# Optimization experiments

Hardware: AMD Instinct MI355X
Metric: run time of the kernel (lower is better)

## Reference

```python
import jax, jax.numpy as jnp
import numpy as np

D, H, DFF, MD = 1024, 16, 4096, 128
B, TS, TT = 8, 512, 512
EPS = 1e-6


def _ln(x, s, b):
    m = jnp.mean(x, axis=-1, keepdims=True)
    v = jnp.mean((x - m) ** 2, axis=-1, keepdims=True)
    return (x - m) * jax.lax.rsqrt(v + EPS) * s + b


def _rel_bias(emb, qlen, klen):
    # T5-style bidirectional bucket: [H, qlen, klen]
    q = jnp.arange(qlen)[:, None]
    k = jnp.arange(klen)[None, :]
    rp = k - q
    bucket = jnp.where(rp < 0, jnp.minimum(-rp, MD - 1), jnp.minimum(rp, MD - 1) + MD)
    return emb[bucket].transpose(2, 0, 1)


def _mha(xq, xkv, w_in, b_in, w_out, b_out, bias):
    # nn.MultiheadAttention math: packed in_proj [3D,D], additive attn bias [H,Tq,Tk]
    Bq, Tq, _ = xq.shape
    Tk = xkv.shape[1]
    hd = D // H
    wq, wk, wv = jnp.split(w_in, 3, axis=0)
    bq, bk, bv = jnp.split(b_in, 3, axis=0)
    q = (xq @ wq.T + bq).reshape(Bq, Tq, H, hd).transpose(0, 2, 1, 3)
    k = (xkv @ wk.T + bk).reshape(Bq, Tk, H, hd).transpose(0, 2, 1, 3)
    v = (xkv @ wv.T + bv).reshape(Bq, Tk, H, hd).transpose(0, 2, 1, 3)
    scores = jnp.einsum('bhqd,bhkd->bhqk', q, k) / jnp.sqrt(jnp.asarray(hd, xq.dtype))
    scores = scores + bias[None]
    attn = jax.nn.softmax(scores, axis=-1)
    out = jnp.einsum('bhqk,bhkd->bhqd', attn, v)
    out = out.transpose(0, 2, 1, 3).reshape(Bq, Tq, D)
    return out @ w_out.T + b_out


def setup_inputs() -> dict:
    key = jax.random.key(0)
    ks = jax.random.split(key, 40)
    std = 0.02

    def n(i, shape):
        return jax.random.normal(ks[i], shape, dtype=jnp.float32) * std

    return {
        'src': jax.random.normal(ks[0], (B, TS, D), dtype=jnp.float32),
        'tgt': jax.random.normal(ks[1], (B, TT, D), dtype=jnp.float32),
        # encoder layer
        'enc_in_w': n(2, (3 * D, D)), 'enc_in_b': jnp.zeros((3 * D,)),
        'enc_out_w': n(3, (D, D)), 'enc_out_b': jnp.zeros((D,)),
        'enc_ff1_w': n(4, (DFF, D)), 'enc_ff1_b': jnp.zeros((DFF,)),
        'enc_ff2_w': n(5, (D, DFF)), 'enc_ff2_b': jnp.zeros((D,)),
        'enc_n1_s': jnp.ones((D,)), 'enc_n1_b': jnp.zeros((D,)),
        'enc_n2_s': jnp.ones((D,)), 'enc_n2_b': jnp.zeros((D,)),
        'enc_rel': n(6, (2 * MD, H)),
        # decoder layer
        'dec_sa_in_w': n(7, (3 * D, D)), 'dec_sa_in_b': jnp.zeros((3 * D,)),
        'dec_sa_out_w': n(8, (D, D)), 'dec_sa_out_b': jnp.zeros((D,)),
        'dec_ca_in_w': n(9, (3 * D, D)), 'dec_ca_in_b': jnp.zeros((3 * D,)),
        'dec_ca_out_w': n(10, (D, D)), 'dec_ca_out_b': jnp.zeros((D,)),
        'dec_ff1_w': n(11, (DFF, D)), 'dec_ff1_b': jnp.zeros((DFF,)),
        'dec_ff2_w': n(12, (D, DFF)), 'dec_ff2_b': jnp.zeros((D,)),
        'dec_n1_s': jnp.ones((D,)), 'dec_n1_b': jnp.zeros((D,)),
        'dec_n2_s': jnp.ones((D,)), 'dec_n2_b': jnp.zeros((D,)),
        'dec_n3_s': jnp.ones((D,)), 'dec_n3_b': jnp.zeros((D,)),
        'dec_rel_self': n(13, (2 * MD, H)),
        'dec_rel_cross': n(14, (2 * MD, H)),
    }


def reference(src, tgt,
              enc_in_w, enc_in_b, enc_out_w, enc_out_b,
              enc_ff1_w, enc_ff1_b, enc_ff2_w, enc_ff2_b,
              enc_n1_s, enc_n1_b, enc_n2_s, enc_n2_b, enc_rel,
              dec_sa_in_w, dec_sa_in_b, dec_sa_out_w, dec_sa_out_b,
              dec_ca_in_w, dec_ca_in_b, dec_ca_out_w, dec_ca_out_b,
              dec_ff1_w, dec_ff1_b, dec_ff2_w, dec_ff2_b,
              dec_n1_s, dec_n1_b, dec_n2_s, dec_n2_b, dec_n3_s, dec_n3_b,
              dec_rel_self, dec_rel_cross):
    Ts, Tt = src.shape[1], tgt.shape[1]

    # ---- encoder layer (pre-LN) ----
    eb = _rel_bias(enc_rel, Ts, Ts)  # [H,Ts,Ts]
    x = src
    x = x + _mha(_ln(x, enc_n1_s, enc_n1_b), _ln(x, enc_n1_s, enc_n1_b),
                 enc_in_w, enc_in_b, enc_out_w, enc_out_b, eb)
    h = _ln(x, enc_n2_s, enc_n2_b)
    x = x + (jax.nn.relu(h @ enc_ff1_w.T + enc_ff1_b) @ enc_ff2_w.T + enc_ff2_b)
    memory = x

    # ---- decoder layer (pre-LN) ----
    causal = jnp.where(jnp.arange(Tt)[None, :] > jnp.arange(Tt)[:, None], -jnp.inf, 0.0)
    sb = _rel_bias(dec_rel_self, Tt, Tt) + causal[None]  # [H,Tt,Tt]
    cb = _rel_bias(dec_rel_cross, Tt, Ts)                # [H,Tt,Ts]
    y = tgt
    yn = _ln(y, dec_n1_s, dec_n1_b)
    y = y + _mha(yn, yn, dec_sa_in_w, dec_sa_in_b, dec_sa_out_w, dec_sa_out_b, sb)
    y = y + _mha(_ln(y, dec_n2_s, dec_n2_b), memory,
                 dec_ca_in_w, dec_ca_in_b, dec_ca_out_w, dec_ca_out_b, cb)
    h = _ln(y, dec_n3_s, dec_n3_b)
    y = y + (jax.nn.relu(h @ dec_ff1_w.T + dec_ff1_b) @ dec_ff2_w.T + dec_ff2_b)
    return y
```

## Files before the change

### kernel.cpp

```cpp
#include <hip/hip_runtime.h>

using u16 = unsigned short;

typedef float f32x4 __attribute__((ext_vector_type(4)));
typedef __bf16 bf16x8v __attribute__((ext_vector_type(8)));
typedef bf16x8v bf16x8 __attribute__((may_alias));
typedef u16 u16x8v __attribute__((ext_vector_type(8)));
typedef u16x8v u16x8 __attribute__((may_alias));
typedef u16 u16x4v __attribute__((ext_vector_type(4)));
typedef u16x4v u16x4 __attribute__((may_alias));
typedef float f32x4v __attribute__((ext_vector_type(4)));
typedef f32x4v float4a __attribute__((may_alias));

#define GPTR(p) ((__attribute__((address_space(1))) void*)(p))
#define LPTR(p) ((__attribute__((address_space(3))) void*)(p))

__device__ __forceinline__ u16 f2bf(float f) {
  unsigned u = __builtin_bit_cast(unsigned, f);
  u += 0x7FFFu + ((u >> 16) & 1u);
  return (u16)(u >> 16);
}

__device__ __forceinline__ f32x4 mfma16(bf16x8 a, bf16x8 b, f32x4 c) {
  return __builtin_amdgcn_mfma_f32_16x16x32_bf16(a, b, c, 0, 0, 0);
}

struct Srcs { const float* s[10]; };

__global__ __launch_bounds__(256) void cvt_all(Srcs srcs, u16* __restrict__ dst) {
  constexpr int off[11] = {0, 786432, 1048576, 2097152, 3145728,
                           3932160, 4194304, 4980736, 5242880, 6291456, 7340032};
  const int i = blockIdx.x * 256 + threadIdx.x;
  int r = 0;
#pragma unroll
  for (int j = 1; j < 10; j++) r += (i >= off[j]);
  float4a v = ((const float4a*)srcs.s[r])[i - off[r]];
  u16x4 o;
  o[0] = f2bf(v[0]); o[1] = f2bf(v[1]); o[2] = f2bf(v[2]); o[3] = f2bf(v[3]);
  ((u16x4*)dst)[i] = o;
}

__global__ __launch_bounds__(256) void add_cvt(const float* __restrict__ a,
                                               const float* __restrict__ b,
                                               u16* __restrict__ o) {
  const int i = blockIdx.x * 256 + threadIdx.x;
  float4a va = ((const float4a*)a)[i];
  float4a vb = ((const float4a*)b)[i];
  u16x4 ov;
#pragma unroll
  for (int j = 0; j < 4; j++) ov[j] = f2bf(va[j] + vb[j]);
  ((u16x4*)o)[i] = ov;
}

__global__ __launch_bounds__(256) void add_f32(float* __restrict__ o,
                                               const float* __restrict__ b) {
  const int i = blockIdx.x * 256 + threadIdx.x;
  float4a vo = ((float4a*)o)[i];
  float4a vb = ((const float4a*)b)[i];
#pragma unroll
  for (int j = 0; j < 4; j++) vo[j] += vb[j];
  ((float4a*)o)[i] = vo;
}

__global__ __launch_bounds__(256) void ln_k(const float* __restrict__ x,
                                            const float* __restrict__ sc,
                                            const float* __restrict__ bi,
                                            u16* __restrict__ out) {
  const int row = blockIdx.x, tid = threadIdx.x;
  float4a v = ((const float4a*)(x + (size_t)row * 1024))[tid];
  float s1 = v[0] + v[1] + v[2] + v[3];
  float s2 = v[0]*v[0] + v[1]*v[1] + v[2]*v[2] + v[3]*v[3];
#pragma unroll
  for (int off = 32; off; off >>= 1) { s1 += __shfl_xor(s1, off); s2 += __shfl_xor(s2, off); }
  __shared__ float red[8];
  if ((tid & 63) == 0) { red[tid >> 6] = s1; red[4 + (tid >> 6)] = s2; }
  __syncthreads();
  s1 = red[0] + red[1] + red[2] + red[3];
  s2 = red[4] + red[5] + red[6] + red[7];
  const float mean = s1 * (1.f / 1024.f);
  const float rstd = rsqrtf(s2 * (1.f / 1024.f) - mean * mean + 1e-6f);
  float4a s4 = ((const float4a*)sc)[tid];
  float4a b4 = ((const float4a*)bi)[tid];
  u16x4 o;
#pragma unroll
  for (int j = 0; j < 4; j++) o[j] = f2bf((v[j] - mean) * rstd * s4[j] + b4[j]);
  ((u16x4*)(out + (size_t)row * 1024))[tid] = o;
}

template <int BN_T, int MW, int EPI, int PF>
__global__ __launch_bounds__(256) void gemm_bt(
    const u16* __restrict__ A, int lda,
    const u16* __restrict__ W, int ldw,
    const float* __restrict__ bias,
    const float* __restrict__ C0, int ldc0,
    void* __restrict__ outv, int ldo, int K,
    float* __restrict__ part) {
  constexpr int BM = 128, BK = 64;
  constexpr int NW = 4 / MW;
  constexpr int FM = BM / MW / 16;
  constexpr int FN = BN_T / NW / 16;
  constexpr int RA = (BM * BK * 2) / 4096;
  constexpr int RB = (BN_T * BK * 2) / 4096;
  constexpr int NB = PF ? 2 : 1;
  __shared__ alignas(16) u16 As[NB][BM * BK];
  __shared__ alignas(16) u16 Bs[NB][BN_T * BK];
  const int tid = threadIdx.x, lane = tid & 63, wv = tid >> 6;
  const int kb = (EPI == 3) ? blockIdx.z * K : 0;

  const int gx = gridDim.x;
  const int nwg = gx * gridDim.y;
  const int orig = blockIdx.y * gx + blockIdx.x;
  const int qq = nwg >> 3, rr = nwg & 7;
  const int xcd = orig & 7, idx = orig >> 3;
  const int wg = (xcd < rr ? xcd * (qq + 1) : rr * (qq + 1) + (xcd - rr) * qq) + idx;
  const int bm = (wg / gx) * BM, bn = (wg % gx) * BN_T;

  const int wr = (wv / NW) * (BM / MW);
  const int wc = (wv % NW) * (BN_T / NW);
  const int la = lane & 15, lg = lane >> 4;
  const int r7 = la & 7;
  const int srow = wv * 8 + (lane >> 3);
  const int scol = ((lane & 7) ^ (lane >> 3)) << 3;
  const u16* gA = A + (size_t)(bm + srow) * lda + scol;
  const u16* gB = W + (size_t)(bn + srow) * ldw + scol;

  f32x4 acc[FM][FN] = {};

  auto stage = [&](int buf, int k0) {
#pragma unroll
    for (int r = 0; r < RA; r++)
      __builtin_amdgcn_global_load_lds(GPTR(gA + (size_t)r * 32 * lda + k0),
                                       LPTR(&As[buf][(wv * 8 + r * 32) * BK]), 16, 0, 0);
#pragma unroll
    for (int r = 0; r < RB; r++)
      __builtin_amdgcn_global_load_lds(GPTR(gB + (size_t)r * 32 * ldw + k0),
                                       LPTR(&Bs[buf][(wv * 8 + r * 32) * BK]), 16, 0, 0);
  };

  auto compute = [&](int buf) {
#pragma unroll
    for (int kk = 0; kk < BK; kk += 32) {
      const int off = ((((kk >> 3) + lg) ^ r7) << 3);
      bf16x8 af[FM], bfr[FN];
#pragma unroll
      for (int m = 0; m < FM; m++)
        af[m] = *(const bf16x8*)&As[buf][(wr + m * 16 + la) * BK + off];
#pragma unroll
      for (int n = 0; n < FN; n++)
        bfr[n] = *(const bf16x8*)&Bs[buf][(wc + n * 16 + la) * BK + off];
#pragma unroll
      for (int m = 0; m < FM; m++)
#pragma unroll
        for (int n = 0; n < FN; n++)
          acc[m][n] = mfma16(af[m], bfr[n], acc[m][n]);
    }
  };

  if constexpr (PF) {
    stage(0, kb);
    int buf = 0;
    const int NT = K / BK;
    for (int t = 0; t < NT; ++t) {
      if (t + 1 < NT) {
        stage(buf ^ 1, kb + (t + 1) * BK);
        if constexpr (RA + RB == 8)
          asm volatile("s_waitcnt vmcnt(8)" ::: "memory");
        else
          asm volatile("s_waitcnt vmcnt(6)" ::: "memory");
      } else {
        asm volatile("s_waitcnt vmcnt(0)" ::: "memory");
      }
      __builtin_amdgcn_s_barrier();
      __builtin_amdgcn_sched_barrier(0);
      compute(buf);
      __builtin_amdgcn_s_barrier();
      buf ^= 1;
    }
  } else {
    for (int k0 = 0; k0 < K; k0 += BK) {
      __syncthreads();
      stage(0, kb + k0);
      __syncthreads();
      compute(0);
    }
  }

  const bool addb = (EPI != 3) || (blockIdx.z == 0);
  float bv[FN];
#pragma unroll
  for (int n = 0; n < FN; n++) bv[n] = addb ? bias[bn + wc + n * 16 + la] : 0.f;
#pragma unroll
  for (int m = 0; m < FM; m++) {
#pragma unroll
    for (int j = 0; j < 4; j++) {
      const int row = bm + wr + m * 16 + (lane >> 4) * 4 + j;
#pragma unroll
      for (int n = 0; n < FN; n++) {
        const int col = bn + wc + n * 16 + la;
        float v = acc[m][n][j] + bv[n];
        if constexpr (EPI == 1) v = fmaxf(v, 0.f);
        if constexpr (EPI == 2) {
          ((float*)outv)[(size_t)row * ldo + col] = v + C0[(size_t)row * ldc0 + col];
        } else if constexpr (EPI == 3) {
          if (blockIdx.z == 0)
            ((float*)outv)[(size_t)row * ldo + col] = v + C0[(size_t)row * ldc0 + col];
          else
            part[(size_t)row * ldo + col] = v;
        } else {
          ((u16*)outv)[(size_t)row * ldo + col] = f2bf(v);
        }
      }
    }
  }
}

template <bool CAUSAL>
__global__ __launch_bounds__(256) void attn_k(
    const u16* __restrict__ Qb, int ldq,
    const u16* __restrict__ Kb, int ldk,
    const u16* __restrict__ Vb, int ldv,
    const float* __restrict__ rel,
    u16* __restrict__ Ob, int ldo,
    int Tq, int Tk) {
  __shared__ alignas(16) u16 Ks[128 * 64];
  __shared__ alignas(16) u16 Vt[64 * 136];
  __shared__ alignas(16) u16 Ps[4][16 * 40];
  __shared__ float biasl[256];
  const int tid = threadIdx.x, lane = tid & 63, w = tid >> 6;
  const int b = blockIdx.y >> 4, h = blockIdx.y & 15;
  const int q0 = blockIdx.x * 64;
  const int la = lane & 15, lg = lane >> 4, r7 = la & 7;

  biasl[tid] = rel[tid * 16 + h];

  const int qr0 = q0 + w * 16;
  const u16* qp = Qb + (size_t)(b * Tq + qr0 + la) * ldq + h * 64 + lg * 8;
  const bf16x8 qf0 = *(const bf16x8*)qp;
  const bf16x8 qf1 = *(const bf16x8*)(qp + 32);

  float sm[4] = {0.f, 0.f, 0.f, 0.f};
  f32x4 acc[4] = {};

  const int kv_end = CAUSAL ? (q0 + 64) : Tk;
  const int scolK = ((lane & 7) ^ (lane >> 3)) << 3;
  const u16* gK = Kb + (size_t)(b * Tk + w * 8 + (lane >> 3)) * ldk + h * 64 + scolK;
  const int vrow = tid >> 3;
  const int vcol = (tid & 7) * 8;
  const int vsw = (tid & 3) * 8;
  const u16* gV = Vb + (size_t)(b * Tk + vrow) * ldv + h * 64 + vcol;
  u16* Pw = Ps[w];

  for (int kv0 = 0; kv0 < kv_end; kv0 += 128) {
    __syncthreads();
#pragma unroll
    for (int r = 0; r < 4; r++)
      __builtin_amdgcn_global_load_lds(GPTR(gK + (size_t)(kv0 + r * 32) * ldk),
                                       LPTR(&Ks[(w * 8 + r * 32) * 64]), 16, 0, 0);
    u16x8 vreg[4];
#pragma unroll
    for (int r = 0; r < 4; r++)
      vreg[r] = *(const u16x8*)(gV + (size_t)(kv0 + r * 32) * ldv);
    asm volatile("s_waitcnt vmcnt(0)" ::: "memory");
#pragma unroll
    for (int r = 0; r < 4; r++) {
      const int rsw = (r * 32 + vrow) ^ vsw;
#pragma unroll
      for (int j = 0; j < 8; j++) Vt[(vcol + j) * 136 + rsw] = vreg[r][j];
    }
    __syncthreads();

#pragma unroll
    for (int sIdx = 0; sIdx < 4; sIdx++) {
#pragma unroll
      for (int half = 0; half < 2; half++) {
        const int kvt = sIdx * 2 + half;
        const bf16x8 kf0 = *(const bf16x8*)&Ks[(kvt * 16 + la) * 64 + ((lg ^ r7) << 3)];
        const bf16x8 kf1 = *(const bf16x8*)&Ks[(kvt * 16 + la) * 64 + (((4 + lg) ^ r7) << 3)];
        f32x4 t2 = {};
        t2 = mfma16(qf0, kf0, t2);
        t2 = mfma16(qf1, kf1, t2);
        const int kc = kv0 + kvt * 16 + la;
#pragma unroll
        for (int j = 0; j < 4; j++) {
          const int qr = qr0 + lg * 4 + j;
          const int rp = kc - qr;
          const int bucket = rp < 0 ? (rp > -127 ? -rp : 127) : (rp < 127 ? rp : 127) + 128;
          float sv = t2[j] * 0.125f + biasl[bucket];
          if (CAUSAL && kc > qr) sv = -30.f;
          const float p = __expf(sv);
          sm[j] += p;
          Pw[(lg * 4 + j) * 40 + half * 16 + la] = f2bf(p);
        }
      }
      const bf16x8 pf = *(const bf16x8*)&Pw[la * 40 + lg * 8];
#pragma unroll
      for (int n = 0; n < 4; n++) {
        const int dd = n * 16 + la;
        const int cc = (sIdx * 32 + lg * 8) ^ (((dd >> 3) & 3) * 8);
        const bf16x8 vf = *(const bf16x8*)&Vt[dd * 136 + cc];
        acc[n] = mfma16(pf, vf, acc[n]);
      }
    }
  }
#pragma unroll
  for (int j = 0; j < 4; j++) {
#pragma unroll
    for (int off = 1; off < 16; off <<= 1) sm[j] += __shfl_xor(sm[j], off);
  }
#pragma unroll
  for (int n = 0; n < 4; n++)
#pragma unroll
    for (int j = 0; j < 4; j++) {
      const int qr = qr0 + lg * 4 + j;
      Ob[(size_t)(b * Tq + qr) * ldo + h * 64 + n * 16 + la] = f2bf(acc[n][j] / sm[j]);
    }
}

extern "C" void kernel_launch(void* const* d_in, const int* in_sizes, int n_in,
                              void* d_out, int out_size, void* d_ws, size_t ws_size,
                              hipStream_t stream) {
  (void)in_sizes; (void)n_in; (void)out_size; (void)ws_size;
  const float* src       = (const float*)d_in[0];
  const float* tgt       = (const float*)d_in[1];
  const float* enc_in_w  = (const float*)d_in[2];
  const float* enc_in_b  = (const float*)d_in[3];
  const float* enc_out_w = (const float*)d_in[4];
  const float* enc_out_b = (const float*)d_in[5];
  const float* enc_ff1_w = (const float*)d_in[6];
  const float* enc_ff1_b = (const float*)d_in[7];
  const float* enc_ff2_w = (const float*)d_in[8];
  const float* enc_ff2_b = (const float*)d_in[9];
  const float* enc_n1_s  = (const float*)d_in[10];
  const float* enc_n1_b  = (const float*)d_in[11];
  const float* enc_n2_s  = (const float*)d_in[12];
  const float* enc_n2_b  = (const float*)d_in[13];
  const float* enc_rel   = (const float*)d_in[14];
  const float* dsa_in_w  = (const float*)d_in[15];
  const float* dsa_in_b  = (const float*)d_in[16];
  const float* dsa_out_w = (const float*)d_in[17];
  const float* dsa_out_b = (const float*)d_in[18];
  const float* dca_in_w  = (const float*)d_in[19];
  const float* dca_in_b  = (const float*)d_in[20];
  const float* dca_out_w = (const float*)d_in[21];
  const float* dca_out_b = (const float*)d_in[22];
  const float* dff1_w    = (const float*)d_in[23];
  const float* dff1_b    = (const float*)d_in[24];
  const float* dff2_w    = (const float*)d_in[25];
  const float* dff2_b    = (const float*)d_in[26];
  const float* dn1_s     = (const float*)d_in[27];
  const float* dn1_b     = (const float*)d_in[28];
  const float* dn2_s     = (const float*)d_in[29];
  const float* dn2_b     = (const float*)d_in[30];
  const float* dn3_s     = (const float*)d_in[31];
  const float* dn3_b     = (const float*)d_in[32];
  const float* drel_s    = (const float*)d_in[33];
  const float* drel_c    = (const float*)d_in[34];
  float* fo = (float*)d_out;

  char* w8 = (char*)d_ws;
  float* x_ws  = (float*)(w8 + 0);
  u16* ln_buf  = (u16*)(w8 + 16777216);
  u16* qkv     = (u16*)(w8 + 25165824);
  u16* attn_o  = (u16*)(w8 + 50331648);
  u16* ffh     = qkv;
  u16* memb    = (u16*)(w8 + 58720256);
  u16* wb      = (u16*)(w8 + 67108864);

  u16* w_enc_in  = wb;
  u16* w_enc_out = wb + 3145728;
  u16* w_enc_f1  = wb + 4194304;
  u16* w_enc_f2  = wb + 8388608;
  u16* w_dsa_in  = wb + 12582912;
  u16* w_dsa_out = wb + 15728640;
  u16* w_dca_in  = wb + 16777216;
  u16* w_dca_out = wb + 19922944;
  u16* w_dff1    = wb + 20971520;
  u16* w_dff2    = wb + 25165824;

  Srcs srcs = {{enc_in_w, enc_out_w, enc_ff1_w, enc_ff2_w, dsa_in_w,
                dsa_out_w, dca_in_w, dca_out_w, dff1_w, dff2_w}};
  cvt_all<<<dim3(28672), 256, 0, stream>>>(srcs, wb);

  ln_k<<<dim3(4096), 256, 0, stream>>>(src, enc_n1_s, enc_n1_b, ln_buf);
  gemm_bt<128,2,0,0><<<dim3(24, 32), 256, 0, stream>>>(ln_buf, 1024, w_enc_in, 1024, enc_in_b, nullptr, 0, qkv, 3072, 1024, nullptr);
  attn_k<false><<<dim3(8, 128), 256, 0, stream>>>(qkv, 3072, qkv + 1024, 3072, qkv + 2048, 3072, enc_rel, attn_o, 1024, 512, 512);
  gemm_bt<64,4,2,1><<<dim3(16, 32), 256, 0, stream>>>(attn_o, 1024, w_enc_out, 1024, enc_out_b, src, 1024, x_ws, 1024, 1024, nullptr);
  ln_k<<<dim3(4096), 256, 0, stream>>>(x_ws, enc_n2_s, enc_n2_b, ln_buf);
  gemm_bt<128,2,1,0><<<dim3(32, 32), 256, 0, stream>>>(ln_buf, 1024, w_enc_f1, 1024, enc_ff1_b, nullptr, 0, ffh, 4096, 1024, nullptr);
  gemm_bt<128,2,3,1><<<dim3(8, 32, 2), 256, 0, stream>>>(ffh, 4096, w_enc_f2, 4096, enc_ff2_b, x_ws, 1024, x_ws, 1024, 2048, fo);
  add_cvt<<<dim3(4096), 256, 0, stream>>>(x_ws, fo, memb);

  ln_k<<<dim3(4096), 256, 0, stream>>>(tgt, dn1_s, dn1_b, ln_buf);
  gemm_bt<128,2,0,0><<<dim3(24, 32), 256, 0, stream>>>(ln_buf, 1024, w_dsa_in, 1024, dsa_in_b, nullptr, 0, qkv, 3072, 1024, nullptr);
  attn_k<true><<<dim3(8, 128), 256, 0, stream>>>(qkv, 3072, qkv + 1024, 3072, qkv + 2048, 3072, drel_s, attn_o, 1024, 512, 512);
  gemm_bt<64,4,2,1><<<dim3(16, 32), 256, 0, stream>>>(attn_o, 1024, w_dsa_out, 1024, dsa_out_b, tgt, 1024, fo, 1024, 1024, nullptr);

  ln_k<<<dim3(4096), 256, 0, stream>>>(fo, dn2_s, dn2_b, ln_buf);
  gemm_bt<64,4,0,1><<<dim3(16, 32), 256, 0, stream>>>(ln_buf, 1024, w_dca_in, 1024, dca_in_b, nullptr, 0, qkv, 3072, 1024, nullptr);
  gemm_bt<128,2,0,0><<<dim3(16, 32), 256, 0, stream>>>(memb, 1024, w_dca_in + 1048576, 1024, dca_in_b + 1024, nullptr, 0, qkv + 1024, 3072, 1024, nullptr);
  attn_k<false><<<dim3(8, 128), 256, 0, stream>>>(qkv, 3072, qkv + 1024, 3072, qkv + 2048, 3072, drel_c, attn_o, 1024, 512, 512);
  gemm_bt<64,4,2,1><<<dim3(16, 32), 256, 0, stream>>>(attn_o, 1024, w_dca_out, 1024, dca_out_b, fo, 1024, fo, 1024, 1024, nullptr);

  ln_k<<<dim3(4096), 256, 0, stream>>>(fo, dn3_s, dn3_b, ln_buf);
  gemm_bt<128,2,1,0><<<dim3(32, 32), 256, 0, stream>>>(ln_buf, 1024, w_dff1, 1024, dff1_b, nullptr, 0, ffh, 4096, 1024, nullptr);
  gemm_bt<128,2,3,1><<<dim3(8, 32, 2), 256, 0, stream>>>(ffh, 4096, w_dff2, 4096, dff2_b, fo, 1024, fo, 1024, 2048, x_ws);
  add_f32<<<dim3(4096), 256, 0, stream>>>(fo, x_ws);
}
```

Measured before the change: 585.2 us.

## Add 256x256-tile double-buffered GEMM with XCD remap for FFN1 layers

```diff
diff --git a/kernel.cpp b/kernel.cpp
--- a/kernel.cpp
+++ b/kernel.cpp
@@ -212,6 +212,123 @@
       }
     }
   }
+}
+
+__global__ __launch_bounds__(512) void gemm256_relu(
+    const u16* __restrict__ A, int lda,
+    const u16* __restrict__ W, int ldw,
+    const float* __restrict__ bias,
+    u16* __restrict__ out, int ldo, int K) {
+  __shared__ alignas(16) u16 As[2][256 * 64];
+  __shared__ alignas(16) u16 Bs[2][256 * 64];
+  const int tid = threadIdx.x, lane = tid & 63, wid = tid >> 6;
+  const int wm = wid >> 2, wn = wid & 3;
+  const int gx = gridDim.x;
+  const int nwg = gx * gridDim.y;
+  const int orig = blockIdx.y * gx + blockIdx.x;
+  const int qq = nwg >> 3, rr = nwg & 7;
+  const int xcd = orig & 7, idx = orig >> 3;
+  const int wg = (xcd < rr ? xcd * (qq + 1) : rr * (qq + 1) + (xcd - rr) * qq) + idx;
+  const int bm = (wg / gx) * 256, bn = (wg % gx) * 256;
+
+  const int la = lane & 15, lg = lane >> 4, r7 = la & 7;
+  const int srow = tid >> 3;
+  const int scol = ((tid & 7) ^ (srow & 7)) << 3;
+  const u16* gA = A + (size_t)(bm + srow) * lda + scol;
+  const u16* gB = W + (size_t)(bn + srow) * ldw + scol;
+
+  f32x4 acc[8][4] = {};
+
+#define STG(ARR, GP, LD, buf, k0, h)                                               \
+  {                                                                                \
+    _Pragma("unroll")                                                              \
+    for (int r = 2 * (h); r < 2 * (h) + 2; r++)                                    \
+      __builtin_amdgcn_global_load_lds(GPTR(GP + (size_t)(r * 64) * LD + (k0)),    \
+                                       LPTR(&ARR[buf][(r * 64 + wid * 8) * 64]),   \
+                                       16, 0, 0);                                  \
+  }
+#define RDB(buf, kk)                                                               \
+  _Pragma("unroll")                                                                \
+  for (int nf = 0; nf < 4; nf++)                                                   \
+    Br[nf] = *(const bf16x8*)&Bs[buf][(wn * 64 + nf * 16 + la) * 64 +              \
+                                      (((((kk) >> 3) + lg) ^ r7) << 3)];
+#define RDA(buf, kk, mh)                                                           \
+  _Pragma("unroll")                                                                \
+  for (int mi = 0; mi < 4; mi++)                                                   \
+    Ar[mi] = *(const bf16x8*)&As[buf][(wm * 128 + ((mh) * 4 + mi) * 16 + la) * 64 +\
+                                      (((((kk) >> 3) + lg) ^ r7) << 3)];
+#define MM(mh)                                                                     \
+  __builtin_amdgcn_s_barrier();                                                    \
+  asm volatile("s_waitcnt lgkmcnt(0)" ::: "memory");                               \
+  __builtin_amdgcn_sched_barrier(0);                                               \
+  __builtin_amdgcn_s_setprio(1);                                                   \
+  _Pragma("unroll")                                                                \
+  for (int mi = 0; mi < 4; mi++)                                                   \
+    _Pragma("unroll")                                                              \
+    for (int nf = 0; nf < 4; nf++)                                                 \
+      acc[(mh) * 4 + mi][nf] = mfma16(Ar[mi], Br[nf], acc[(mh) * 4 + mi][nf]);     \
+  __builtin_amdgcn_s_setprio(0);                                                   \
+  __builtin_amdgcn_s_barrier();
+
+  STG(As, gA, lda, 0, 0, 0) STG(As, gA, lda, 0, 0, 1)
+  STG(Bs, gB, ldw, 0, 0, 0) STG(Bs, gB, ldw, 0, 0, 1)
+  asm volatile("s_waitcnt vmcnt(0)" ::: "memory");
+  __builtin_amdgcn_s_barrier();
+
+  const int NIT = K >> 7;
+  for (int it = 0; it < NIT; ++it) {
+    const int k1 = it * 128 + 64;
+    const int k2 = it * 128 + 128;
+    const bool more = (it + 1 < NIT);
+    bf16x8 Ar[4], Br[4];
+
+    RDB(0, 0) RDA(0, 0, 0) STG(As, gA, lda, 1, k1, 0)
+    __builtin_amdgcn_sched_barrier(0);
+    MM(0)
+    RDA(0, 0, 1) STG(As, gA, lda, 1, k1, 1)
+    __builtin_amdgcn_sched_barrier(0);
+    MM(1)
+    RDB(0, 32) RDA(0, 32, 1) STG(Bs, gB, ldw, 1, k1, 0)
+    __builtin_amdgcn_sched_barrier(0);
+    MM(1)
+    RDA(0, 32, 0) STG(Bs, gB, ldw, 1, k1, 1)
+    __builtin_amdgcn_sched_barrier(0);
+    asm volatile("s_waitcnt vmcnt(0)" ::: "memory");
+    MM(0)
+    RDB(1, 0) RDA(1, 0, 0) if (more) STG(As, gA, lda, 0, k2, 0)
+    __builtin_amdgcn_sched_barrier(0);
+    MM(0)
+    RDA(1, 0, 1) if (more) STG(As, gA, lda, 0, k2, 1)
+    __builtin_amdgcn_sched_barrier(0);
+    MM(1)
+    RDB(1, 32) RDA(1, 32, 1) if (more) STG(Bs, gB, ldw, 0, k2, 0)
+    __builtin_amdgcn_sched_barrier(0);
+    MM(1)
+    RDA(1, 32, 0) if (more) STG(Bs, gB, ldw, 0, k2, 1)
+    __builtin_amdgcn_sched_barrier(0);
+    if (more) { asm volatile("s_waitcnt vmcnt(0)" ::: "memory"); }
+    MM(0)
+  }
+#undef STG
+#undef RDB
+#undef RDA
+#undef MM
+
+  float bv[4];
+#pragma unroll
+  for (int nf = 0; nf < 4; nf++) bv[nf] = bias[bn + wn * 64 + nf * 16 + la];
+#pragma unroll
+  for (int mf = 0; mf < 8; mf++)
+#pragma unroll
+    for (int j = 0; j < 4; j++) {
+      const int row = bm + wm * 128 + mf * 16 + lg * 4 + j;
+#pragma unroll
+      for (int nf = 0; nf < 4; nf++) {
+        const int col = bn + wn * 64 + nf * 16 + la;
+        float v = fmaxf(acc[mf][nf][j] + bv[nf], 0.f);
+        out[(size_t)row * ldo + col] = f2bf(v);
+      }
+    }
 }
 
 template <bool CAUSAL>
@@ -386,7 +503,7 @@
   attn_k<false><<<dim3(8, 128), 256, 0, stream>>>(qkv, 3072, qkv + 1024, 3072, qkv + 2048, 3072, enc_rel, attn_o, 1024, 512, 512);
   gemm_bt<64,4,2,1><<<dim3(16, 32), 256, 0, stream>>>(attn_o, 1024, w_enc_out, 1024, enc_out_b, src, 1024, x_ws, 1024, 1024, nullptr);
   ln_k<<<dim3(4096), 256, 0, stream>>>(x_ws, enc_n2_s, enc_n2_b, ln_buf);
-  gemm_bt<128,2,1,0><<<dim3(32, 32), 256, 0, stream>>>(ln_buf, 1024, w_enc_f1, 1024, enc_ff1_b, nullptr, 0, ffh, 4096, 1024, nullptr);
+  gemm256_relu<<<dim3(16, 16), 512, 0, stream>>>(ln_buf, 1024, w_enc_f1, 1024, enc_ff1_b, ffh, 4096, 1024);
   gemm_bt<128,2,3,1><<<dim3(8, 32, 2), 256, 0, stream>>>(ffh, 4096, w_enc_f2, 4096, enc_ff2_b, x_ws, 1024, x_ws, 1024, 2048, fo);
   add_cvt<<<dim3(4096), 256, 0, stream>>>(x_ws, fo, memb);
 
@@ -402,7 +519,7 @@
   gemm_bt<64,4,2,1><<<dim3(16, 32), 256, 0, stream>>>(attn_o, 1024, w_dca_out, 1024, dca_out_b, fo, 1024, fo, 1024, 1024, nullptr);
 
   ln_k<<<dim3(4096), 256, 0, stream>>>(fo, dn3_s, dn3_b, ln_buf);
-  gemm_bt<128,2,1,0><<<dim3(32, 32), 256, 0, stream>>>(ln_buf, 1024, w_dff1, 1024, dff1_b, nullptr, 0, ffh, 4096, 1024, nullptr);
+  gemm256_relu<<<dim3(16, 16), 512, 0, stream>>>(ln_buf, 1024, w_dff1, 1024, dff1_b, ffh, 4096, 1024);
   gemm_bt<128,2,3,1><<<dim3(8, 32, 2), 256, 0, stream>>>(ffh, 4096, w_dff2, 4096, dff2_b, fo, 1024, fo, 1024, 2048, x_ws);
   add_f32<<<dim3(4096), 256, 0, stream>>>(fo, x_ws);
 }
```

Result: no change. 576.9 us (-1.4%).
